# Optimization experiments

Hardware: AMD Instinct MI355X
Metric: run time of the kernel (lower is better)

The kernel has to match this reference:

```python
import jax, jax.numpy as jnp
import numpy as np

NUM_HEADS = 8      # in_channels // num_head_channels = 512 // 64
NUM_GROUPS = 32    # GroupNorm groups
EPS = 1e-5


def setup_inputs() -> dict:
    key = jax.random.key(0)
    ks = jax.random.split(key, 6)
    C = 512
    x = jax.random.normal(ks[0], (8, C, 32, 32), dtype=jnp.float32)
    gn_w = jax.random.normal(ks[1], (C,), dtype=jnp.float32) * 0.1 + 1.0
    gn_b = jax.random.normal(ks[2], (C,), dtype=jnp.float32) * 0.1
    qkv_w = jax.random.normal(ks[3], (3 * C, C), dtype=jnp.float32) / np.sqrt(C)
    qkv_b = jnp.zeros((3 * C,), dtype=jnp.float32)
    # NOTE: original zero-initializes to_out; we use small random weights so the
    # attention path contributes to the output (math is identical).
    out_w = jax.random.normal(ks[4], (C, C), dtype=jnp.float32) * 0.02
    out_b = jax.random.normal(ks[5], (C,), dtype=jnp.float32) * 0.02
    return {"x": x, "gn_w": gn_w, "gn_b": gn_b, "qkv_w": qkv_w,
            "qkv_b": qkv_b, "out_w": out_w, "out_b": out_b}


def _group_norm(net, gn_w, gn_b):
    b, c, t = net.shape
    g = net.reshape(b, NUM_GROUPS, c // NUM_GROUPS, t)
    mu = jnp.mean(g, axis=(2, 3), keepdims=True)
    var = jnp.var(g, axis=(2, 3), keepdims=True)
    n = ((g - mu) * jax.lax.rsqrt(var + EPS)).reshape(b, c, t)
    return n * gn_w[None, :, None] + gn_b[None, :, None]


def reference(x, gn_w, gn_b, qkv_w, qkv_b, out_w, out_b):
    b, c, h, w = x.shape
    area = h * w
    inp = x.reshape(b, c, area)                      # [b, c, t]
    n = _group_norm(inp, gn_w, gn_b)
    # 1x1 conv1d == channel GEMM
    qkv = jnp.einsum('oc,bct->bot', qkv_w, n) + qkv_b[None, :, None]  # [b, 3c, t]
    hd = c // NUM_HEADS
    # split_qkv_after_heads: view(b*H, 3*hd, area) then split along channel
    qkv = qkv.reshape(b * NUM_HEADS, 3 * hd, area)
    q, k, v = qkv[:, :hd], qkv[:, hd:2 * hd], qkv[:, 2 * hd:]
    scale = 1.0 / np.sqrt(np.sqrt(hd))               # sqrt-sqrt per-tensor scale
    attn = jnp.einsum('bct,bcs->bts', q * scale, k * scale)  # [bH, t, s]
    prob = jax.nn.softmax(attn, axis=-1)
    net = jnp.einsum('bts,bcs->bct', prob, v).reshape(b, c, area)
    out = jnp.einsum('oc,bct->bot', out_w, net) + out_b[None, :, None]
    return (inp + out).reshape(b, c, h, w)
```

## Files before the change

kernel.cpp:

```cpp
#include <hip/hip_runtime.h>
#include <hip/hip_bf16.h>

typedef __bf16 bf16_t;
typedef __bf16 bf16x8 __attribute__((ext_vector_type(8)));
typedef __bf16 bf16x4 __attribute__((ext_vector_type(4)));
typedef short  s16x4  __attribute__((ext_vector_type(4)));
typedef float  f32x4  __attribute__((ext_vector_type(4)));

#define B_DIM 8
#define C_DIM 512
#define T_DIM 1024
#define NH 8
#define HD 64

__device__ __forceinline__ f32x4 mfma16_bf16(bf16x4 a, bf16x4 b, f32x4 c) {
    return __builtin_amdgcn_mfma_f32_16x16x16bf16_1k(
        __builtin_bit_cast(s16x4, a), __builtin_bit_cast(s16x4, b), c, 0, 0, 0);
}

__global__ __launch_bounds__(256) void prep_w(const float* __restrict__ w1,
                                              const float* __restrict__ w2,
                                              bf16_t* __restrict__ o1,
                                              bf16_t* __restrict__ o2)
{
    int tid = blockIdx.x * 256 + threadIdx.x;
    for (int p = 0; p < 4; ++p) {
        int q = tid + p * 65536;
        const f32x4* src;
        bf16x4* dst;
        int qq;
        if (q < 196608) { src = (const f32x4*)w1; dst = (bf16x4*)o1; qq = q; }
        else            { src = (const f32x4*)w2; dst = (bf16x4*)o2; qq = q - 196608; }
        f32x4 f = src[qq];
        bf16x4 h;
        for (int j = 0; j < 4; ++j) h[j] = (bf16_t)f[j];
        dst[qq] = h;
    }
}

__global__ __launch_bounds__(256) void gn_kernel(const float* __restrict__ x,
                                                 const float* __restrict__ gw,
                                                 const float* __restrict__ gb,
                                                 bf16_t* __restrict__ n_t)
{
    __shared__ bf16_t sX[16384];
    __shared__ float sred[8];
    int tid = threadIdx.x;
    int bb  = blockIdx.x >> 5;
    int g   = blockIdx.x & 31;
    const f32x4* xg4 = reinterpret_cast<const f32x4*>(x + (size_t)(bb * C_DIM + g * 16) * T_DIM);

    float s = 0.f, sq = 0.f;
    for (int i = 0; i < 16; ++i) {
        int v = tid + i * 256;
        f32x4 f = xg4[v];
        bf16x4 h;
        for (int j = 0; j < 4; ++j) {
            s += f[j]; sq += f[j] * f[j];
            h[j] = (bf16_t)f[j];
        }
        *reinterpret_cast<bf16x4*>(sX + v * 4) = h;
    }
    for (int off = 1; off < 64; off <<= 1) {
        s  += __shfl_xor(s, off);
        sq += __shfl_xor(sq, off);
    }
    int wv = tid >> 6;
    if ((tid & 63) == 0) { sred[wv * 2] = s; sred[wv * 2 + 1] = sq; }
    __syncthreads();
    s  = sred[0] + sred[2] + sred[4] + sred[6];
    sq = sred[1] + sred[3] + sred[5] + sred[7];
    float mean = s * (1.f / 16384.f);
    float var  = sq * (1.f / 16384.f) - mean * mean;
    float rs   = rsqrtf(var + 1e-5f);

    int hf = tid & 1;
    float aa[8], bbias[8];
    for (int j = 0; j < 8; ++j) {
        int c = hf * 8 + j;
        float av = gw[g * 16 + c] * rs;
        aa[j] = av;
        bbias[j] = gb[g * 16 + c] - mean * av;
    }
    bf16_t* ob = n_t + (size_t)bb * T_DIM * C_DIM + g * 16 + hf * 8;
    for (int p = 0; p < 8; ++p) {
        int t = (tid >> 1) + p * 128;
        bf16x8 o;
        for (int j = 0; j < 8; ++j) {
            float xv = (float)sX[(hf * 8 + j) * 1024 + t];
            o[j] = (bf16_t)(xv * aa[j] + bbias[j]);
        }
        *reinterpret_cast<bf16x8*>(ob + (size_t)t * C_DIM) = o;
    }
}

__global__ __launch_bounds__(256) void qkv_gemm_kernel(
    const bf16_t* __restrict__ wqb, const float* __restrict__ bq,
    const bf16_t* __restrict__ n_t, bf16_t* __restrict__ qkv)
{
    __shared__ bf16_t sA[64 * 72];
    __shared__ bf16_t sB[128 * 72];
    int tid = threadIdx.x;
    int w = tid >> 6, lane = tid & 63, quad = lane >> 4, l15 = lane & 15;
    int bx = blockIdx.x;
    int t0 = blockIdx.y * 128;
    int bb = blockIdx.z;
    int o0 = bx * 64;
    const bf16_t* Ab = wqb + (size_t)o0 * C_DIM;
    const bf16_t* Bb = n_t + ((size_t)bb * T_DIM + t0) * C_DIM;

    f32x4 acc[2][4];
    for (int mt = 0; mt < 2; ++mt)
        for (int nt = 0; nt < 4; ++nt)
            acc[mt][nt] = f32x4{0.f, 0.f, 0.f, 0.f};
    int mw0 = (w >> 1) * 32;
    int nw0 = (w & 1) * 64;

    for (int k0 = 0; k0 < C_DIM; k0 += 64) {
        for (int i = 0; i < 2; ++i) {
            int v = tid + i * 256;
            int row = v >> 3, c8 = v & 7;
            *reinterpret_cast<bf16x8*>(sA + row * 72 + c8 * 8) =
                *reinterpret_cast<const bf16x8*>(Ab + (size_t)row * C_DIM + k0 + c8 * 8);
        }
        for (int i = 0; i < 4; ++i) {
            int v = tid + i * 256;
            int row = v >> 3, c8 = v & 7;
            *reinterpret_cast<bf16x8*>(sB + row * 72 + c8 * 8) =
                *reinterpret_cast<const bf16x8*>(Bb + (size_t)row * C_DIM + k0 + c8 * 8);
        }
        __syncthreads();
        for (int kk = 0; kk < 2; ++kk) {
            bf16x8 af[2], bfr[4];
            for (int mt = 0; mt < 2; ++mt)
                af[mt] = *reinterpret_cast<const bf16x8*>(sA + (mw0 + mt * 16 + l15) * 72 + kk * 32 + quad * 8);
            for (int nt = 0; nt < 4; ++nt)
                bfr[nt] = *reinterpret_cast<const bf16x8*>(sB + (nw0 + nt * 16 + l15) * 72 + kk * 32 + quad * 8);
            for (int mt = 0; mt < 2; ++mt)
                for (int nt = 0; nt < 4; ++nt)
                    acc[mt][nt] = __builtin_amdgcn_mfma_f32_16x16x32_bf16(af[mt], bfr[nt], acc[mt][nt], 0, 0, 0);
        }
        __syncthreads();
    }

    int h = bx / 3, type = bx % 3;
    size_t base = ((size_t)(bb * NH + h) * 3 + type) * (64 * 1024);

    if (type < 2) {
        for (int mt = 0; mt < 2; ++mt)
            for (int nt = 0; nt < 4; ++nt)
                for (int r = 0; r < 4; ++r) {
                    int mw = mw0 + mt * 16 + quad * 4 + r;
                    int tl = nw0 + nt * 16 + l15;
                    float v = acc[mt][nt][r] + bq[o0 + mw];
                    sB[tl * 72 + mw] = (bf16_t)v;
                }
        __syncthreads();
        for (int i = 0; i < 4; ++i) {
            int v = tid + i * 256;
            int tl = v >> 3, c8 = v & 7;
            bf16x8 d = *reinterpret_cast<const bf16x8*>(sB + tl * 72 + c8 * 8);
            *reinterpret_cast<bf16x8*>(qkv + base + (size_t)(t0 + tl) * 64 + c8 * 8) = d;
        }
    } else {
        for (int mt = 0; mt < 2; ++mt)
            for (int nt = 0; nt < 4; ++nt)
                for (int r = 0; r < 4; ++r) {
                    int mw = mw0 + mt * 16 + quad * 4 + r;
                    int tl = nw0 + nt * 16 + l15;
                    float v = acc[mt][nt][r] + bq[o0 + mw];
                    sB[mw * 136 + tl] = (bf16_t)v;
                }
        __syncthreads();
        for (int i = 0; i < 4; ++i) {
            int v = tid + i * 256;
            int cc = v >> 4, t8 = (v & 15) * 8;
            bf16x8 d = *reinterpret_cast<const bf16x8*>(sB + cc * 136 + t8);
            *reinterpret_cast<bf16x8*>(qkv + base + (size_t)cc * 1024 + t0 + t8) = d;
        }
    }
}

__global__ __launch_bounds__(256, 6) void attn_kernel(const bf16_t* __restrict__ qkv,
                                                      bf16_t* __restrict__ net_t)
{
    __shared__ bf16_t sK[64 * 72];
    __shared__ bf16_t sV[64 * 72];
    int tid = threadIdx.x;
    int w = tid >> 6, lane = tid & 63, quad = lane >> 4, l15 = lane & 15;
    int bh = blockIdx.x;
    int qt = blockIdx.y;
    size_t qb = (size_t)bh * 3 * 65536;
    const bf16_t* Qg = qkv + qb + (size_t)qt * 4096;
    const bf16_t* Kg = qkv + qb + 65536;
    const bf16_t* Vg = qkv + qb + 2 * 65536;
    const float K2 = 0.125f * 1.44269504088896f;

    bf16x8 qf[2];
    for (int kk = 0; kk < 2; ++kk)
        qf[kk] = *reinterpret_cast<const bf16x8*>(Qg + (size_t)(w * 16 + l15) * 64 + kk * 32 + quad * 8);

    bf16x8 kreg[2], vreg[2];
    for (int i = 0; i < 2; ++i) {
        int v = tid + i * 256;
        kreg[i] = *reinterpret_cast<const bf16x8*>(Kg + (size_t)(v >> 3) * 64 + (v & 7) * 8);
        vreg[i] = *reinterpret_cast<const bf16x8*>(Vg + (size_t)(v >> 3) * 1024 + (v & 7) * 8);
    }

    f32x4 O[4];
    for (int i = 0; i < 4; ++i) O[i] = f32x4{0.f, 0.f, 0.f, 0.f};
    float lsum = 0.f;

    for (int st = 0; st < 16; ++st) {
        __syncthreads();
        for (int i = 0; i < 2; ++i) {
            int v = tid + i * 256;
            *reinterpret_cast<bf16x8*>(sK + (v >> 3) * 72 + (v & 7) * 8) = kreg[i];
            *reinterpret_cast<bf16x8*>(sV + (v >> 3) * 72 + (v & 7) * 8) = vreg[i];
        }
        __syncthreads();
        if (st < 15) {
            int s0n = (st + 1) * 64;
            for (int i = 0; i < 2; ++i) {
                int v = tid + i * 256;
                kreg[i] = *reinterpret_cast<const bf16x8*>(Kg + (size_t)(s0n + (v >> 3)) * 64 + (v & 7) * 8);
                vreg[i] = *reinterpret_cast<const bf16x8*>(Vg + (size_t)(v >> 3) * 1024 + s0n + (v & 7) * 8);
            }
        }

        for (int mt = 0; mt < 4; ++mt) {
            f32x4 S = f32x4{0.f, 0.f, 0.f, 0.f};
            for (int kk = 0; kk < 2; ++kk) {
                bf16x8 kf = *reinterpret_cast<const bf16x8*>(sK + (mt * 16 + l15) * 72 + kk * 32 + quad * 8);
                S = __builtin_amdgcn_mfma_f32_16x16x32_bf16(kf, qf[kk], S, 0, 0, 0);
            }
            bf16x4 pf;
            for (int r = 0; r < 4; ++r) {
                float p = exp2f(S[r] * K2);
                lsum += p;
                pf[r] = (bf16_t)p;
            }
            for (int ct = 0; ct < 4; ++ct) {
                bf16x4 vf = *reinterpret_cast<const bf16x4*>(sV + (ct * 16 + l15) * 72 + mt * 16 + quad * 4);
                O[ct] = mfma16_bf16(vf, pf, O[ct]);
            }
        }
    }

    lsum += __shfl_xor(lsum, 16);
    lsum += __shfl_xor(lsum, 32);
    float inv = 1.f / lsum;

    int bb = bh >> 3, h = bh & 7;
    int t = qt * 64 + w * 16 + l15;
    bf16_t* orow = net_t + ((size_t)bb * T_DIM + t) * C_DIM + h * 64;
    for (int ct = 0; ct < 4; ++ct) {
        bf16x4 o4;
        for (int r = 0; r < 4; ++r) o4[r] = (bf16_t)(O[ct][r] * inv);
        *reinterpret_cast<bf16x4*>(orow + ct * 16 + quad * 4) = o4;
    }
}

__global__ __launch_bounds__(256) void out_gemm_kernel(
    const bf16_t* __restrict__ wob, const float* __restrict__ bo,
    const bf16_t* __restrict__ net_t, const float* __restrict__ x,
    float* __restrict__ out)
{
    __shared__ bf16_t sA[64 * 72];
    __shared__ bf16_t sB[128 * 72];
    int tid = threadIdx.x;
    int w = tid >> 6, lane = tid & 63, quad = lane >> 4, l15 = lane & 15;
    int o0 = blockIdx.x * 64;
    int t0 = blockIdx.y * 128;
    int bb = blockIdx.z;
    const bf16_t* Ab = wob + (size_t)o0 * C_DIM;
    const bf16_t* Bb = net_t + ((size_t)bb * T_DIM + t0) * C_DIM;

    f32x4 acc[2][4];
    for (int mt = 0; mt < 2; ++mt)
        for (int nt = 0; nt < 4; ++nt)
            acc[mt][nt] = f32x4{0.f, 0.f, 0.f, 0.f};
    int mw0 = (w >> 1) * 32;
    int nw0 = (w & 1) * 64;

    for (int k0 = 0; k0 < C_DIM; k0 += 64) {
        for (int i = 0; i < 2; ++i) {
            int v = tid + i * 256;
            int row = v >> 3, c8 = v & 7;
            *reinterpret_cast<bf16x8*>(sA + row * 72 + c8 * 8) =
                *reinterpret_cast<const bf16x8*>(Ab + (size_t)row * C_DIM + k0 + c8 * 8);
        }
        for (int i = 0; i < 4; ++i) {
            int v = tid + i * 256;
            int row = v >> 3, c8 = v & 7;
            *reinterpret_cast<bf16x8*>(sB + row * 72 + c8 * 8) =
                *reinterpret_cast<const bf16x8*>(Bb + (size_t)row * C_DIM + k0 + c8 * 8);
        }
        __syncthreads();
        for (int kk = 0; kk < 2; ++kk) {
            bf16x8 af[2], bfr[4];
            for (int mt = 0; mt < 2; ++mt)
                af[mt] = *reinterpret_cast<const bf16x8*>(sA + (mw0 + mt * 16 + l15) * 72 + kk * 32 + quad * 8);
            for (int nt = 0; nt < 4; ++nt)
                bfr[nt] = *reinterpret_cast<const bf16x8*>(sB + (nw0 + nt * 16 + l15) * 72 + kk * 32 + quad * 8);
            for (int mt = 0; mt < 2; ++mt)
                for (int nt = 0; nt < 4; ++nt)
                    acc[mt][nt] = __builtin_amdgcn_mfma_f32_16x16x32_bf16(af[mt], bfr[nt], acc[mt][nt], 0, 0, 0);
        }
        __syncthreads();
    }

    for (int mt = 0; mt < 2; ++mt)
        for (int nt = 0; nt < 4; ++nt)
            for (int r = 0; r < 4; ++r) {
                int o = o0 + mw0 + mt * 16 + quad * 4 + r;
                int t = t0 + nw0 + nt * 16 + l15;
                size_t idx = ((size_t)bb * C_DIM + o) * T_DIM + t;
                out[idx] = acc[mt][nt][r] + bo[o] + x[idx];
            }
}

extern "C" void kernel_launch(void* const* d_in, const int* in_sizes, int n_in,
                              void* d_out, int out_size, void* d_ws, size_t ws_size,
                              hipStream_t stream)
{
    const float* x     = (const float*)d_in[0];
    const float* gn_w  = (const float*)d_in[1];
    const float* gn_b  = (const float*)d_in[2];
    const float* qkv_w = (const float*)d_in[3];
    const float* qkv_b = (const float*)d_in[4];
    const float* out_w = (const float*)d_in[5];
    const float* out_b = (const float*)d_in[6];
    float* out = (float*)d_out;

    char* ws = (char*)d_ws;
    bf16_t* n_t   = (bf16_t*)(ws);
    bf16_t* qkv   = (bf16_t*)(ws + 8388608);
    bf16_t* net_t = (bf16_t*)(ws + 33554432);
    bf16_t* wqb   = (bf16_t*)(ws + 41943040);
    bf16_t* wob   = (bf16_t*)(ws + 41943040 + 1572864);

    prep_w<<<dim3(256), 256, 0, stream>>>(qkv_w, out_w, wqb, wob);
    gn_kernel<<<dim3(256), 256, 0, stream>>>(x, gn_w, gn_b, n_t);
    qkv_gemm_kernel<<<dim3(24, 8, 8), 256, 0, stream>>>(wqb, qkv_b, n_t, qkv);
    attn_kernel<<<dim3(64, 16), 256, 0, stream>>>(qkv, net_t);
    out_gemm_kernel<<<dim3(8, 8, 8), 256, 0, stream>>>(wob, out_b, net_t, x, out);
}
```

Measured before the change: 162.9 us.

## Double-buffer K/V LDS tiles in attention and fold softmax scale into Q

Folds the softmax scale and log2e factor into Q when the QKV GEMM writes it out, so attention can call the raw exp2 builtin without a multiply. The attention kernel now ping-pongs two LDS buffers for K/V, cutting the barriers per tile and overlapping global loads with compute. It raises wave priority around the MFMA work and computes the row sum with an MFMA against a vector of ones instead of scalar adds plus shuffles. The extra LDS and registers lower the occupancy bound from 6 to 4 blocks, and rounding the scaled Q to bf16 slightly changes numerics.

Result: faster. 157.1 us (-3.6%).

```diff
diff --git a/kernel.cpp b/kernel.cpp
--- a/kernel.cpp
+++ b/kernel.cpp
@@ -13,9 +13,16 @@
 #define NH 8
 #define HD 64
 
+#define QSCALE 0.180336880111112f
+
 __device__ __forceinline__ f32x4 mfma16_bf16(bf16x4 a, bf16x4 b, f32x4 c) {
     return __builtin_amdgcn_mfma_f32_16x16x16bf16_1k(
         __builtin_bit_cast(s16x4, a), __builtin_bit_cast(s16x4, b), c, 0, 0, 0);
+}
+
+__device__ __forceinline__ void block_sync_lds() {
+    asm volatile("s_waitcnt lgkmcnt(0)" ::: "memory");
+    __builtin_amdgcn_s_barrier();
 }
 
 __global__ __launch_bounds__(256) void prep_w(const float* __restrict__ w1,
@@ -147,12 +154,13 @@
     size_t base = ((size_t)(bb * NH + h) * 3 + type) * (64 * 1024);
 
     if (type < 2) {
+        float scl = (type == 0) ? QSCALE : 1.0f;
         for (int mt = 0; mt < 2; ++mt)
             for (int nt = 0; nt < 4; ++nt)
                 for (int r = 0; r < 4; ++r) {
                     int mw = mw0 + mt * 16 + quad * 4 + r;
                     int tl = nw0 + nt * 16 + l15;
-                    float v = acc[mt][nt][r] + bq[o0 + mw];
+                    float v = (acc[mt][nt][r] + bq[o0 + mw]) * scl;
                     sB[tl * 72 + mw] = (bf16_t)v;
                 }
         __syncthreads();
@@ -181,11 +189,13 @@
     }
 }
 
-__global__ __launch_bounds__(256, 6) void attn_kernel(const bf16_t* __restrict__ qkv,
+__global__ __launch_bounds__(256, 4) void attn_kernel(const bf16_t* __restrict__ qkv,
                                                       bf16_t* __restrict__ net_t)
 {
-    __shared__ bf16_t sK[64 * 72];
-    __shared__ bf16_t sV[64 * 72];
+    __shared__ bf16_t sK0[64 * 72];
+    __shared__ bf16_t sV0[64 * 72];
+    __shared__ bf16_t sK1[64 * 72];
+    __shared__ bf16_t sV1[64 * 72];
     int tid = threadIdx.x;
     int w = tid >> 6, lane = tid & 63, quad = lane >> 4, l15 = lane & 15;
     int bh = blockIdx.x;
@@ -194,62 +204,75 @@
     const bf16_t* Qg = qkv + qb + (size_t)qt * 4096;
     const bf16_t* Kg = qkv + qb + 65536;
     const bf16_t* Vg = qkv + qb + 2 * 65536;
-    const float K2 = 0.125f * 1.44269504088896f;
 
     bf16x8 qf[2];
     for (int kk = 0; kk < 2; ++kk)
         qf[kk] = *reinterpret_cast<const bf16x8*>(Qg + (size_t)(w * 16 + l15) * 64 + kk * 32 + quad * 8);
 
-    bf16x8 kreg[2], vreg[2];
-    for (int i = 0; i < 2; ++i) {
-        int v = tid + i * 256;
-        kreg[i] = *reinterpret_cast<const bf16x8*>(Kg + (size_t)(v >> 3) * 64 + (v & 7) * 8);
-        vreg[i] = *reinterpret_cast<const bf16x8*>(Vg + (size_t)(v >> 3) * 1024 + (v & 7) * 8);
-    }
+    int vrow = tid >> 3;
+    int vcol = (tid & 7) * 8;
+
+    bf16x8 kA[2], vA[2], kB[2], vB[2];
+
+    auto load_tiles = [&](bf16x8* kr, bf16x8* vr, int s0) {
+        for (int i = 0; i < 2; ++i) {
+            int r = vrow + i * 32;
+            kr[i] = *reinterpret_cast<const bf16x8*>(Kg + (size_t)(s0 + r) * 64 + vcol);
+            vr[i] = *reinterpret_cast<const bf16x8*>(Vg + (size_t)r * 1024 + s0 + vcol);
+        }
+    };
+    auto write_tiles = [&](bf16_t* sKb, bf16_t* sVb, const bf16x8* kr, const bf16x8* vr) {
+        for (int i = 0; i < 2; ++i) {
+            int r = vrow + i * 32;
+            *reinterpret_cast<bf16x8*>(sKb + r * 72 + vcol) = kr[i];
+            *reinterpret_cast<bf16x8*>(sVb + r * 72 + vcol) = vr[i];
+        }
+    };
 
     f32x4 O[4];
     for (int i = 0; i < 4; ++i) O[i] = f32x4{0.f, 0.f, 0.f, 0.f};
-    float lsum = 0.f;
-
-    for (int st = 0; st < 16; ++st) {
-        __syncthreads();
-        for (int i = 0; i < 2; ++i) {
-            int v = tid + i * 256;
-            *reinterpret_cast<bf16x8*>(sK + (v >> 3) * 72 + (v & 7) * 8) = kreg[i];
-            *reinterpret_cast<bf16x8*>(sV + (v >> 3) * 72 + (v & 7) * 8) = vreg[i];
-        }
-        __syncthreads();
-        if (st < 15) {
-            int s0n = (st + 1) * 64;
-            for (int i = 0; i < 2; ++i) {
-                int v = tid + i * 256;
-                kreg[i] = *reinterpret_cast<const bf16x8*>(Kg + (size_t)(s0n + (v >> 3)) * 64 + (v & 7) * 8);
-                vreg[i] = *reinterpret_cast<const bf16x8*>(Vg + (size_t)(v >> 3) * 1024 + s0n + (v & 7) * 8);
-            }
-        }
-
+    f32x4 L = f32x4{0.f, 0.f, 0.f, 0.f};
+    const bf16x4 kONES = bf16x4{(bf16_t)1.f, (bf16_t)1.f, (bf16_t)1.f, (bf16_t)1.f};
+
+    auto compute_tile = [&](const bf16_t* sKb, const bf16_t* sVb) {
+        __builtin_amdgcn_s_setprio(1);
         for (int mt = 0; mt < 4; ++mt) {
             f32x4 S = f32x4{0.f, 0.f, 0.f, 0.f};
             for (int kk = 0; kk < 2; ++kk) {
-                bf16x8 kf = *reinterpret_cast<const bf16x8*>(sK + (mt * 16 + l15) * 72 + kk * 32 + quad * 8);
+                bf16x8 kf = *reinterpret_cast<const bf16x8*>(sKb + (mt * 16 + l15) * 72 + kk * 32 + quad * 8);
                 S = __builtin_amdgcn_mfma_f32_16x16x32_bf16(kf, qf[kk], S, 0, 0, 0);
             }
             bf16x4 pf;
-            for (int r = 0; r < 4; ++r) {
-                float p = exp2f(S[r] * K2);
-                lsum += p;
-                pf[r] = (bf16_t)p;
-            }
+            for (int r = 0; r < 4; ++r)
+                pf[r] = (bf16_t)__builtin_amdgcn_exp2f(S[r]);
+            L = mfma16_bf16(kONES, pf, L);
             for (int ct = 0; ct < 4; ++ct) {
-                bf16x4 vf = *reinterpret_cast<const bf16x4*>(sV + (ct * 16 + l15) * 72 + mt * 16 + quad * 4);
+                bf16x4 vf = *reinterpret_cast<const bf16x4*>(sVb + (ct * 16 + l15) * 72 + mt * 16 + quad * 4);
                 O[ct] = mfma16_bf16(vf, pf, O[ct]);
             }
         }
-    }
-
-    lsum += __shfl_xor(lsum, 16);
-    lsum += __shfl_xor(lsum, 32);
-    float inv = 1.f / lsum;
+        __builtin_amdgcn_s_setprio(0);
+    };
+
+    load_tiles(kA, vA, 0);
+    write_tiles(sK0, sV0, kA, vA);
+    load_tiles(kB, vB, 64);
+    block_sync_lds();
+
+    for (int st2 = 0; st2 < 8; ++st2) {
+        write_tiles(sK1, sV1, kB, vB);
+        if (st2 < 7) load_tiles(kA, vA, (2 * st2 + 2) * 64);
+        compute_tile(sK0, sV0);
+        block_sync_lds();
+        if (st2 < 7) {
+            write_tiles(sK0, sV0, kA, vA);
+            load_tiles(kB, vB, (2 * st2 + 3) * 64);
+        }
+        compute_tile(sK1, sV1);
+        if (st2 < 7) block_sync_lds();
+    }
+
+    float inv = 1.f / L[0];
 
     int bb = bh >> 3, h = bh & 7;
     int t = qt * 64 + w * 16 + l15;
```
